# Kernel tuning notes

Measured on AMD Instinct MI355X. Metric: run time of the kernel, lower is better.

## Reference

```python
import jax, jax.numpy as jnp
import numpy as np

B, N, M = 8, 4096, 4096

def _sqdist(x, y):
    # x: [B,N,3], y: [B,M,3] -> squared euclidean distances [B,N,M]
    return jnp.sum((x[:, :, None, :] - y[:, None, :, :]) ** 2, axis=-1)

def _approx_match(xyz1, xyz2):
    # Faithful port of Fan et al. approxmatch.cu (used by PyTorchEMD's
    # earth_mover_distance): annealed soft-assignment over 10 levels.
    b, n, _ = xyz1.shape
    m = xyz2.shape[1]
    d2 = _sqdist(xyz1, xyz2)                      # [B,N,M]
    factorl = max(n, m) / n
    factorr = max(n, m) / m
    satl = jnp.full((b, n), factorl, d2.dtype)    # remaining mass, left
    satr = jnp.full((b, m), factorr, d2.dtype)    # remaining mass, right
    match = jnp.zeros_like(d2)
    # levels: -4^7 .. -4^-1, then 0 (exactly as in approxmatch.cu)
    levels = [-(4.0 ** j) for j in range(7, -2, -1)] + [0.0]
    for level in levels:
        w = jnp.exp(level * d2) * satr[:, None, :]                 # [B,N,M]
        w = w * (satl / (jnp.sum(w, axis=2) + 1e-9))[:, :, None]   # row normalize
        ss2 = jnp.sum(w, axis=1)                                   # [B,M]
        ratio = jnp.minimum(satr / (ss2 + 1e-9), 1.0)
        w = w * ratio[:, None, :]                                  # col capacity clamp
        match = match + w
        satl = jnp.maximum(satl - jnp.sum(w, axis=2), 0.0)
        satr = jnp.maximum(satr - ss2 * ratio, 0.0)
    return match, d2

def setup_inputs() -> dict:
    key = jax.random.key(0)
    k1, k2 = jax.random.split(key)
    array1 = jax.random.uniform(k1, (B, N, 3), dtype=jnp.float32)
    array2 = jax.random.uniform(k2, (B, M, 3), dtype=jnp.float32)
    return {"array1": array1, "array2": array2}

def reference(array1, array2):
    match, d2 = _approx_match(array1, array2)
    dist = jnp.sum(match * d2, axis=(1, 2))   # per-batch EMD (squared-dist transport cost), [B]
    return jnp.mean(dist) / array1.shape[1]
```

## Files before the change

### kernel.cpp

```cpp
#include <hip/hip_runtime.h>


#define BB 8
#define NN 4096
#define MM 4096
#define NPTS 4096

constexpr int   BLK   = 256;
constexpr int   S     = 16;
constexpr int   R     = 4;
constexpr int   RPB   = (BLK / S) * R;
constexpr int   CHUNK = 2048;
constexpr int   G     = (CHUNK / S) / 4;
constexpr float TAU   = 1e-8f;

#if defined(__has_builtin)
#if __has_builtin(__builtin_amdgcn_exp2f)
#define EXP2F(x) __builtin_amdgcn_exp2f(x)
#endif
#if __has_builtin(__builtin_amdgcn_logf)
#define LOG2F(x) __builtin_amdgcn_logf(x)
#endif
#endif
#ifndef EXP2F
#define EXP2F(x) exp2f(x)
#endif
#ifndef LOG2F
#define LOG2F(x) log2f(x)
#endif

__global__ void emd_sort(const float* __restrict__ xyz, float* __restrict__ xyzs) {
    __shared__ int hist[64];
    __shared__ int cur[64];
    const int b = blockIdx.x;
    const float* src = xyz + (size_t)b * NPTS * 3;
    float* dst = xyzs + (size_t)b * NPTS * 3;
    for (int i = threadIdx.x; i < 64; i += BLK) hist[i] = 0;
    __syncthreads();
    for (int i = threadIdx.x; i < NPTS; i += BLK) {
        float x = src[3*i], y = src[3*i+1], z = src[3*i+2];
        int cx = (int)(x * 4.0f); cx = cx < 0 ? 0 : (cx > 3 ? 3 : cx);
        int cy = (int)(y * 4.0f); cy = cy < 0 ? 0 : (cy > 3 ? 3 : cy);
        int cz = (int)(z * 4.0f); cz = cz < 0 ? 0 : (cz > 3 ? 3 : cz);
        atomicAdd(&hist[(cx << 4) | (cy << 2) | cz], 1);
    }
    __syncthreads();
    if (threadIdx.x == 0) {
        int acc = 0;
        for (int k = 0; k < 64; ++k) { cur[k] = acc; acc += hist[k]; }
    }
    __syncthreads();
    for (int i = threadIdx.x; i < NPTS; i += BLK) {
        float x = src[3*i], y = src[3*i+1], z = src[3*i+2];
        int cx = (int)(x * 4.0f); cx = cx < 0 ? 0 : (cx > 3 ? 3 : cx);
        int cy = (int)(y * 4.0f); cy = cy < 0 ? 0 : (cy > 3 ? 3 : cy);
        int cz = (int)(z * 4.0f); cz = cz < 0 ? 0 : (cz > 3 ? 3 : cz);
        int idx = atomicAdd(&cur[(cx << 4) | (cy << 2) | cz], 1);
        dst[3*idx] = x; dst[3*idx+1] = y; dst[3*idx+2] = z;
    }
}

__global__ void emd_bbox(const float* __restrict__ xyzs, float* __restrict__ bb,
                         int gp) {
    const int grp = blockIdx.x, lane = threadIdx.x;
    float xlo = 1e30f, xhi = -1e30f, ylo = 1e30f, yhi = -1e30f,
          zlo = 1e30f, zhi = -1e30f;
    if (lane < gp) {
        const float* p = xyzs + ((size_t)grp * gp + lane) * 3;
        xlo = xhi = p[0]; ylo = yhi = p[1]; zlo = zhi = p[2];
    }
    #pragma unroll
    for (int d = 1; d < 64; d <<= 1) {
        xlo = fminf(xlo, __shfl_xor(xlo, d)); xhi = fmaxf(xhi, __shfl_xor(xhi, d));
        ylo = fminf(ylo, __shfl_xor(ylo, d)); yhi = fmaxf(yhi, __shfl_xor(yhi, d));
        zlo = fminf(zlo, __shfl_xor(zlo, d)); zhi = fmaxf(zhi, __shfl_xor(zhi, d));
    }
    if (lane == 0) {
        float* o = bb + (size_t)grp * 6;
        o[0]=xlo; o[1]=xhi; o[2]=ylo; o[3]=yhi; o[4]=zlo; o[5]=zhi;
    }
}

__global__ void emd_init(float* __restrict__ satl, float* __restrict__ satr,
                         float* __restrict__ bsum, float* __restrict__ slsum,
                         float* __restrict__ scal, float* __restrict__ out) {
    int i = blockIdx.x * blockDim.x + threadIdx.x;
    if (i < BB * NN) satl[i] = 1.0f;
    if (i < BB * MM) satr[i] = 1.0f;
    if (i < BB)      bsum[i] = 0.0f;
    if (i < BB)      slsum[i] = 0.0f;
    if (i < BB * 5)  scal[i] = 0.0f;
    if (i == 0)      out[0]  = 0.0f;
}

__global__ void compact_rows(const float* __restrict__ xyzs,
                             const float* __restrict__ satl,
                             float* __restrict__ sl,
                             float4* __restrict__ rowBuf, int* __restrict__ rIdx,
                             int* __restrict__ rCnt) {
    __shared__ int cnts[BLK];
    const int b = blockIdx.x;
    const int PER = NN / BLK;
    const float* sb  = satl + (size_t)b * NN;
    float*       slb = sl   + (size_t)b * NN;
    const float* xb  = xyzs + (size_t)b * NN * 3;
    const int st = threadIdx.x * PER;
    int c = 0;
    for (int i = 0; i < PER; ++i) c += (sb[st + i] > TAU) ? 1 : 0;
    cnts[threadIdx.x] = c;
    __syncthreads();
    for (int d = 1; d < BLK; d <<= 1) {
        int v = cnts[threadIdx.x];
        int u = (threadIdx.x >= d) ? cnts[threadIdx.x - d] : 0;
        __syncthreads();
        cnts[threadIdx.x] = v + u;
        __syncthreads();
    }
    const int total = cnts[BLK - 1];
    int off = cnts[threadIdx.x] - c;
    for (int i = 0; i < PER; ++i) {
        int n = st + i;
        if (sb[n] > TAU) {
            rowBuf[(size_t)b * NN + off] =
                make_float4(xb[3*n], xb[3*n+1], xb[3*n+2], slb[n]);
            rIdx[(size_t)b * NN + off] = n;
            ++off;
        } else if (slb[n] != 0.0f) {
            slb[n] = 0.0f;
        }
    }
    for (int i = total + threadIdx.x; i < NN; i += BLK) {
        rowBuf[(size_t)b * NN + i] = make_float4(0.f, 0.f, 0.f, 0.f);
        rIdx[(size_t)b * NN + i] = 0;
    }
    if (threadIdx.x == 0) rCnt[b] = total;
}

__global__ void compact_cols(const float* __restrict__ xyzs,
                             const float* __restrict__ satr,
                             float4* __restrict__ colBuf, int* __restrict__ cIdx,
                             int* __restrict__ cCnt) {
    __shared__ int cnts[BLK];
    const int b = blockIdx.x;
    const int PER = MM / BLK;
    const float* sb = satr + (size_t)b * MM;
    const float* xb = xyzs + (size_t)b * MM * 3;
    const int st = threadIdx.x * PER;
    int c = 0;
    for (int i = 0; i < PER; ++i) c += (sb[st + i] > TAU) ? 1 : 0;
    cnts[threadIdx.x] = c;
    __syncthreads();
    for (int d = 1; d < BLK; d <<= 1) {
        int v = cnts[threadIdx.x];
        int u = (threadIdx.x >= d) ? cnts[threadIdx.x - d] : 0;
        __syncthreads();
        cnts[threadIdx.x] = v + u;
        __syncthreads();
    }
    const int total = cnts[BLK - 1];
    int off = cnts[threadIdx.x] - c;
    for (int i = 0; i < PER; ++i) {
        int m = st + i;
        if (sb[m] > TAU) {
            colBuf[(size_t)b * MM + off] =
                make_float4(xb[3*m], xb[3*m+1], xb[3*m+2], sb[m]);
            cIdx[(size_t)b * MM + off] = m;
            ++off;
        }
    }
    for (int i = total + threadIdx.x; i < MM; i += BLK) {
        colBuf[(size_t)b * MM + i] = make_float4(0.f, 0.f, 0.f, 0.f);
        cIdx[(size_t)b * MM + i] = 0;
    }
    if (threadIdx.x == 0) cCnt[b] = total;
}

#define AB_LOAD(vv, gg)                                          \
    _Pragma("unroll")                                            \
    for (int k = 0; k < 4; ++k) vv[k] = q[((gg)*4 + k)*S + s];

#define AB_COMP(vv)                                              \
    _Pragma("unroll")                                            \
    for (int k = 0; k < 4; ++k) {                                \
        float4 v = vv[k];                                        \
        _Pragma("unroll")                                        \
        for (int r = 0; r < R; ++r) {                            \
            float a0 = v.w + cpp[r];                             \
            float a1 = fmaf(zs[r], v.z, a0);                     \
            float a2 = fmaf(ys[r], v.y, a1);                     \
            float arg = fmaf(xs[r], v.x, a2);                    \
            acc[r] += EXP2F(arg);                                \
        }                                                        \
    }

#define RED_S(v)                                                 \
    v += __shfl_xor(v, 1);  v += __shfl_xor(v, 2);               \
    v += __shfl_xor(v, 4);  v += __shfl_xor(v, 8);

#define RED_W(v)                                                 \
    v += __shfl_xor(v, 1);  v += __shfl_xor(v, 2);               \
    v += __shfl_xor(v, 4);  v += __shfl_xor(v, 8);               \
    v += __shfl_xor(v, 16); v += __shfl_xor(v, 32);

#define BOX_SETUP(rbb)                                           \
    const float* rb = (rbb) + (size_t)(b * 256 + tile * 4 + (threadIdx.x >> 6)) * 6; \
    const float rx0 = rb[0], rx1 = rb[1], ry0 = rb[2], ry1 = rb[3], \
                rz0 = rb[4], rz1 = rb[5];

#define BOX_D2M(cbb, c0, gs, d2m)                                \
    const float* cb = (cbb) + (size_t)(b * 64 + ((c0) >> 6) + (gs)) * 6; \
    float gx = fmaxf(0.0f, fmaxf(cb[0] - rx1, rx0 - cb[1]));     \
    float gy = fmaxf(0.0f, fmaxf(cb[2] - ry1, ry0 - cb[3]));     \
    float gz = fmaxf(0.0f, fmaxf(cb[4] - rz1, rz0 - cb[5]));     \
    float d2m = fmaf(gx, gx, fmaf(gy, gy, gz * gz));

__global__ __launch_bounds__(BLK, 2) void emd_passA_p(
        const float* __restrict__ xyz1, const float* __restrict__ xyz2,
        const float* __restrict__ satl, const float* __restrict__ satr,
        float* __restrict__ sl, const float* __restrict__ rbb,
        const float* __restrict__ cbb, float c, float T) {
    __shared__ float4 q[CHUNK];
    const int b    = blockIdx.x / (NN / RPB);
    const int tile = blockIdx.x % (NN / RPB);
    const float* x2b = xyz2 + (size_t)b * MM * 3;
    const float* srb = satr + (size_t)b * MM;

    const int g = threadIdx.x / S, s = threadIdx.x % S;
    const int n0 = tile * RPB + g * R;
    const float* p = xyz1 + ((size_t)b * NN + n0) * 3;
    const float m2c = -2.0f * c;
    float xs[R], ys[R], zs[R], cpp[R], acc[R];
    #pragma unroll
    for (int r = 0; r < R; ++r) {
        float x = p[3*r], y = p[3*r+1], z = p[3*r+2];
        cpp[r] = c * (x*x + y*y + z*z);
        xs[r] = m2c * x; ys[r] = m2c * y; zs[r] = m2c * z;
        acc[r] = 0.0f;
    }
    BOX_SETUP(rbb);

    for (int c0 = 0; c0 < MM; c0 += CHUNK) {
        __syncthreads();
        for (int m = threadIdx.x; m < CHUNK; m += BLK) {
            int mm = c0 + m;
            float xx = x2b[3*mm], yy = x2b[3*mm+1], zz = x2b[3*mm+2];
            float qq = xx*xx + yy*yy + zz*zz;
            q[m] = make_float4(xx, yy, zz, fmaf(c, qq, LOG2F(srb[mm])));
        }
        __syncthreads();
        for (int gs = 0; gs < G; ++gs) {
            BOX_D2M(cbb, c0, gs, d2m);
            if (d2m > T) continue;
            float4 va[4];
            AB_LOAD(va, gs);
            AB_COMP(va);
        }
    }
    #pragma unroll
    for (int r = 0; r < R; ++r) { RED_S(acc[r]); }
    if (s == 0) {
        #pragma unroll
        for (int r = 0; r < R; ++r) {
            int gi = b * NN + n0 + r;
            sl[gi] = satl[gi] / (acc[r] + 1e-9f);
        }
    }
}

__global__ __launch_bounds__(BLK, 2) void emd_passB_p(
        const float* __restrict__ xyz1, const float* __restrict__ xyz2,
        const float* __restrict__ sl, float* __restrict__ satr,
        float* __restrict__ sr2, const float* __restrict__ rbb,
        const float* __restrict__ cbb, float c, float T) {
    __shared__ float4 q[CHUNK];
    const int b    = blockIdx.x / (MM / RPB);
    const int tile = blockIdx.x % (MM / RPB);
    const float* x1b = xyz1 + (size_t)b * NN * 3;
    const float* slb = sl + (size_t)b * NN;

    const int g = threadIdx.x / S, s = threadIdx.x % S;
    const int m0 = tile * RPB + g * R;
    const float* qp = xyz2 + ((size_t)b * MM + m0) * 3;
    const float m2c = -2.0f * c;
    float xs[R], ys[R], zs[R], cpp[R], acc[R];
    #pragma unroll
    for (int r = 0; r < R; ++r) {
        float x = qp[3*r], y = qp[3*r+1], z = qp[3*r+2];
        cpp[r] = c * (x*x + y*y + z*z);
        xs[r] = m2c * x; ys[r] = m2c * y; zs[r] = m2c * z;
        acc[r] = 0.0f;
    }
    BOX_SETUP(rbb);

    for (int c0 = 0; c0 < NN; c0 += CHUNK) {
        __syncthreads();
        for (int n = threadIdx.x; n < CHUNK; n += BLK) {
            int nn = c0 + n;
            float xx = x1b[3*nn], yy = x1b[3*nn+1], zz = x1b[3*nn+2];
            float pp = xx*xx + yy*yy + zz*zz;
            q[n] = make_float4(xx, yy, zz, fmaf(c, pp, LOG2F(slb[nn])));
        }
        __syncthreads();
        for (int gs = 0; gs < G; ++gs) {
            BOX_D2M(cbb, c0, gs, d2m);
            if (d2m > T) continue;
            float4 va[4];
            AB_LOAD(va, gs);
            AB_COMP(va);
        }
    }
    #pragma unroll
    for (int r = 0; r < R; ++r) { RED_S(acc[r]); }
    if (s == 0) {
        #pragma unroll
        for (int r = 0; r < R; ++r) {
            int gi = b * MM + m0 + r;
            float sr    = satr[gi];
            float ss2   = acc[r] * sr;
            float ratio = fminf(sr / (ss2 + 1e-9f), 1.0f);
            float sn    = fmaxf(sr - ss2 * ratio, 0.0f);
            sr2[gi]  = sr * ratio;
            satr[gi] = sn;
        }
    }
}

#define CA0_LOAD(vv, ww, gg)                                     \
    _Pragma("unroll")                                            \
    for (int k = 0; k < 4; ++k) {                                \
        int idx = ((gg)*4 + k)*S + s;                            \
        vv[k] = q[idx]; ww[k] = w[idx];                          \
    }

#define CA0_COMP(vv, ww)                                         \
    _Pragma("unroll")                                            \
    for (int k = 0; k < 4; ++k) {                                \
        float4 v = vv[k]; float2 wv = ww[k];                     \
        _Pragma("unroll")                                        \
        for (int r = 0; r < R; ++r) {                            \
            float a0 = v.w + cnpp[r];                            \
            float a1 = fmaf(zs[r], v.z, a0);                     \
            float a2 = fmaf(ys[r], v.y, a1);                     \
            float arg = fmaf(xs[r], v.x, a2);                    \
            float en  = EXP2F(arg);                              \
            acc2[r] = fmaf(en, wv.y, acc2[r]);                   \
            float e2 = en * en;                                  \
            float t  = (e2 * e2) * wv.x;                         \
            rd[r]   += t;                                        \
            costA[r] = fmaf(t, arg, costA[r]);                   \
        }                                                        \
    }

__global__ __launch_bounds__(BLK, 2) void emd_passCA0_p(
        const float* __restrict__ xyz1, const float* __restrict__ xyz2,
        float* __restrict__ sl, float* __restrict__ satl,
        const float* __restrict__ sr2, const float* __restrict__ satr_next,
        float* __restrict__ out, const float* __restrict__ rbb,
        const float* __restrict__ cbb, float cl, float cn, float T) {
    __shared__ float4 q[CHUNK];
    __shared__ float2 w[CHUNK];
    const int b    = blockIdx.x / (NN / RPB);
    const int tile = blockIdx.x % (NN / RPB);
    const float* x2b = xyz2 + (size_t)b * MM * 3;
    const float* s2b = sr2 + (size_t)b * MM;
    const float* srb = satr_next + (size_t)b * MM;

    const int g = threadIdx.x / S, s = threadIdx.x % S;
    const int n0 = tile * RPB + g * R;
    const float* pp_ = xyz1 + ((size_t)b * NN + n0) * 3;
    const float m2cn = -2.0f * cn;
    const float icn  = 1.0f / cn;
    float xs[R], ys[R], zs[R], cnpp[R], rd[R], costA[R], acc2[R], slv[R];
    #pragma unroll
    for (int r = 0; r < R; ++r) {
        float x = pp_[3*r], y = pp_[3*r+1], z = pp_[3*r+2];
        cnpp[r] = cn * (x*x + y*y + z*z);
        xs[r] = m2cn * x; ys[r] = m2cn * y; zs[r] = m2cn * z;
        rd[r] = 0.0f; costA[r] = 0.0f; acc2[r] = 0.0f;
        slv[r] = sl[b * NN + n0 + r];
    }
    BOX_SETUP(rbb);

    for (int c0 = 0; c0 < MM; c0 += CHUNK) {
        __syncthreads();
        for (int m = threadIdx.x; m < CHUNK; m += BLK) {
            int mm = c0 + m;
            float xx = x2b[3*mm], yy = x2b[3*mm+1], zz = x2b[3*mm+2];
            float qq = xx*xx + yy*yy + zz*zz;
            q[m] = make_float4(xx, yy, zz, cn * qq);
            w[m] = make_float2(s2b[mm], srb[mm]);
        }
        __syncthreads();
        for (int gs = 0; gs < G; ++gs) {
            BOX_D2M(cbb, c0, gs, d2m);
            if (d2m > T) continue;
            float4 va[4]; float2 wa[4];
            CA0_LOAD(va, wa, gs);
            CA0_COMP(va, wa);
        }
    }

    #pragma unroll
    for (int r = 0; r < R; ++r) { RED_S(rd[r]); RED_S(acc2[r]); }

    float csum = 0.0f;
    #pragma unroll
    for (int r = 0; r < R; ++r) csum += (costA[r] * icn) * slv[r];
    RED_W(csum);
    if ((threadIdx.x & 63) == 0)
        atomicAdd(out, csum * (1.0f / (float)(BB * NN)));

    if (s == 0) {
        #pragma unroll
        for (int r = 0; r < R; ++r) {
            int gi = b * NN + n0 + r;
            float sa = fmaxf(satl[gi] - rd[r] * slv[r], 0.0f);
            satl[gi] = sa;
            sl[gi] = sa / (acc2[r] + 1e-9f);
        }
    }
}

__global__ __launch_bounds__(BLK, 2) void emd_passB_c(
        const float4* __restrict__ colBuf, const int* __restrict__ cIdx,
        const int* __restrict__ cCnt, const float4* __restrict__ rowBuf,
        const int* __restrict__ rCnt, float* __restrict__ satr,
        float* __restrict__ sr2c, float* __restrict__ satrnc,
        float* __restrict__ bsum, int do_sum, float c) {
    __shared__ float4 q[CHUNK];
    const int b    = blockIdx.x / (MM / RPB);
    const int tile = blockIdx.x % (MM / RPB);
    const int Mc = cCnt[b], Nc = rCnt[b];
    if (tile * RPB >= Mc) return;
    const float4* rb = rowBuf + (size_t)b * NN;

    const int g = threadIdx.x / S, s = threadIdx.x % S;
    const int m0 = tile * RPB + g * R;
    const float m2c = -2.0f * c;
    float xs[R], ys[R], zs[R], cpp[R], acc[R], srv[R];
    #pragma unroll
    for (int r = 0; r < R; ++r) {
        float4 cv = colBuf[(size_t)b * MM + m0 + r];
        srv[r] = cv.w;
        cpp[r] = c * (cv.x*cv.x + cv.y*cv.y + cv.z*cv.z);
        xs[r] = m2c * cv.x; ys[r] = m2c * cv.y; zs[r] = m2c * cv.z;
        acc[r] = 0.0f;
    }

    const int nch = (Nc + CHUNK - 1) / CHUNK;
    for (int ci = 0; ci < nch; ++ci) {
        const int c0 = ci * CHUNK;
        __syncthreads();
        for (int n = threadIdx.x; n < CHUNK; n += BLK) {
            int nn = c0 + n;
            if (nn < Nc) {
                float4 rv = rb[nn];
                float pp = rv.x*rv.x + rv.y*rv.y + rv.z*rv.z;
                q[n] = make_float4(rv.x, rv.y, rv.z, fmaf(c, pp, LOG2F(rv.w)));
            } else {
                q[n] = make_float4(0.f, 0.f, 0.f, -1e30f);
            }
        }
        __syncthreads();
        int rem = Nc - c0; if (rem > CHUNK) rem = CHUNK;
        const int Gact = (rem + S*4 - 1) / (S*4);
        float4 va[4], vb[4];
        AB_LOAD(va, 0);
        #pragma unroll 1
        for (int gs = 0; gs < Gact; gs += 2) {
            if (gs + 1 < Gact) { AB_LOAD(vb, gs + 1); }
            AB_COMP(va);
            if (gs + 2 < Gact) { AB_LOAD(va, gs + 2); }
            if (gs + 1 < Gact) { AB_COMP(vb); }
        }
    }
    #pragma unroll
    for (int r = 0; r < R; ++r) { RED_S(acc[r]); }
    float part = 0.0f;
    if (s == 0) {
        #pragma unroll
        for (int r = 0; r < R; ++r) {
            if (m0 + r < Mc) {
                float sr    = srv[r];
                float ss2   = acc[r] * sr;
                float ratio = fminf(sr / (ss2 + 1e-9f), 1.0f);
                float sn    = fmaxf(sr - ss2 * ratio, 0.0f);
                size_t ci2 = (size_t)b * MM + m0 + r;
                sr2c[ci2]   = sr * ratio;
                satrnc[ci2] = sn;
                satr[(size_t)b * MM + cIdx[ci2]] = sn;
                part += sn;
            }
        }
    }
    if (do_sum) {
        RED_W(part);
        if ((threadIdx.x & 63) == 0) atomicAdd(&bsum[b], part);
    }
}

__global__ __launch_bounds__(BLK, 2) void emd_passCA0_c(
        const float4* __restrict__ rowBuf, const int* __restrict__ rIdx,
        const int* __restrict__ rCnt, const float4* __restrict__ colBuf,
        const int* __restrict__ cCnt, const float* __restrict__ sr2c,
        const float* __restrict__ satrnc, float* __restrict__ satl,
        float* __restrict__ sl, float* __restrict__ out, float cl, float cn) {
    __shared__ float4 q[CHUNK];
    __shared__ float2 w[CHUNK];
    const int b    = blockIdx.x / (NN / RPB);
    const int tile = blockIdx.x % (NN / RPB);
    const int Nc = rCnt[b], Mc = cCnt[b];
    if (tile * RPB >= Nc) return;
    const float4* cbp = colBuf + (size_t)b * MM;
    const float* s2p = sr2c + (size_t)b * MM;
    const float* snp = satrnc + (size_t)b * MM;

    const int g = threadIdx.x / S, s = threadIdx.x % S;
    const int n0 = tile * RPB + g * R;
    const float m2cn = -2.0f * cn;
    const float icn  = 1.0f / cn;
    float xs[R], ys[R], zs[R], cnpp[R], rd[R], costA[R], acc2[R], slv[R];
    #pragma unroll
    for (int r = 0; r < R; ++r) {
        float4 rv = rowBuf[(size_t)b * NN + n0 + r];
        slv[r] = rv.w;
        cnpp[r] = cn * (rv.x*rv.x + rv.y*rv.y + rv.z*rv.z);
        xs[r] = m2cn * rv.x; ys[r] = m2cn * rv.y; zs[r] = m2cn * rv.z;
        rd[r] = 0.0f; costA[r] = 0.0f; acc2[r] = 0.0f;
    }

    const int nch = (Mc + CHUNK - 1) / CHUNK;
    for (int ci = 0; ci < nch; ++ci) {
        const int c0 = ci * CHUNK;
        __syncthreads();
        for (int m = threadIdx.x; m < CHUNK; m += BLK) {
            int mm = c0 + m;
            if (mm < Mc) {
                float4 cv = cbp[mm];
                float qq = cv.x*cv.x + cv.y*cv.y + cv.z*cv.z;
                q[m] = make_float4(cv.x, cv.y, cv.z, cn * qq);
                w[m] = make_float2(s2p[mm], snp[mm]);
            } else {
                q[m] = make_float4(0.f, 0.f, 0.f, 0.f);
                w[m] = make_float2(0.f, 0.f);
            }
        }
        __syncthreads();
        int rem = Mc - c0; if (rem > CHUNK) rem = CHUNK;
        const int Gact = (rem + S*4 - 1) / (S*4);
        float4 va[4], vb[4]; float2 wa[4], wb[4];
        CA0_LOAD(va, wa, 0);
        #pragma unroll 1
        for (int gs = 0; gs < Gact; gs += 2) {
            if (gs + 1 < Gact) { CA0_LOAD(vb, wb, gs + 1); }
            CA0_COMP(va, wa);
            if (gs + 2 < Gact) { CA0_LOAD(va, wa, gs + 2); }
            if (gs + 1 < Gact) { CA0_COMP(vb, wb); }
        }
    }

    #pragma unroll
    for (int r = 0; r < R; ++r) { RED_S(rd[r]); RED_S(acc2[r]); }

    float csum = 0.0f;
    #pragma unroll
    for (int r = 0; r < R; ++r) csum += (costA[r] * icn) * slv[r];
    RED_W(csum);
    if ((threadIdx.x & 63) == 0)
        atomicAdd(out, csum * (1.0f / (float)(BB * NN)));

    if (s == 0) {
        #pragma unroll
        for (int r = 0; r < R; ++r) {
            if (n0 + r < Nc) {
                int gi = b * NN + rIdx[(size_t)b * NN + n0 + r];
                float sa = fmaxf(satl[gi] - rd[r] * slv[r], 0.0f);
                satl[gi] = sa;
                sl[gi] = sa / (acc2[r] + 1e-9f);
            }
        }
    }
}

#define CA1_LOAD(vv, aa, gg)                                     \
    _Pragma("unroll")                                            \
    for (int k = 0; k < 4; ++k) {                                \
        int idx = ((gg)*4 + k)*S + s;                            \
        vv[k] = q[idx]; aa[k] = qa[idx];                         \
    }

#define CA1_COMP(vv, aa)                                         \
    _Pragma("unroll")                                            \
    for (int k = 0; k < 4; ++k) {                                \
        float4 v = vv[k]; float lw = aa[k];                      \
        _Pragma("unroll")                                        \
        for (int r = 0; r < R; ++r) {                            \
            float a0 = v.w + clpp[r];                            \
            float a1 = fmaf(zs[r], v.z, a0);                     \
            float a2 = fmaf(ys[r], v.y, a1);                     \
            float arg = fmaf(xs[r], v.x, a2);                    \
            float t   = EXP2F(arg);                              \
            rd[r] += t;                                          \
            c1[r] = fmaf(t, arg, c1[r]);                         \
            c2[r] = fmaf(t, lw, c2[r]);                          \
        }                                                        \
    }

__global__ __launch_bounds__(BLK, 2) void emd_passCA1_c(
        const float4* __restrict__ rowBuf, const int* __restrict__ rIdx,
        const int* __restrict__ rCnt, const float4* __restrict__ colBuf,
        const int* __restrict__ cCnt, const float* __restrict__ sr2c,
        float* __restrict__ satl, float* __restrict__ sl,
        const float* __restrict__ bsum, float* __restrict__ slsum,
        float* __restrict__ out, float cl) {
    __shared__ float4 q[CHUNK];
    __shared__ float  qa[CHUNK];
    const int b    = blockIdx.x / (NN / RPB);
    const int tile = blockIdx.x % (NN / RPB);
    const int Nc = rCnt[b], Mc = cCnt[b];
    if (tile * RPB >= Nc) return;
    const float4* cbp = colBuf + (size_t)b * MM;
    const float* s2p = sr2c + (size_t)b * MM;

    const int g = threadIdx.x / S, s = threadIdx.x % S;
    const int n0 = tile * RPB + g * R;
    const float m2cl = -2.0f * cl;
    const float icl  = 1.0f / cl;
    float xs[R], ys[R], zs[R], clpp[R], rd[R], c1[R], c2[R], slv[R];
    #pragma unroll
    for (int r = 0; r < R; ++r) {
        float4 rv = rowBuf[(size_t)b * NN + n0 + r];
        slv[r] = rv.w;
        clpp[r] = cl * (rv.x*rv.x + rv.y*rv.y + rv.z*rv.z);
        xs[r] = m2cl * rv.x; ys[r] = m2cl * rv.y; zs[r] = m2cl * rv.z;
        rd[r] = 0.0f; c1[r] = 0.0f; c2[r] = 0.0f;
    }

    const int nch = (Mc + CHUNK - 1) / CHUNK;
    for (int ci = 0; ci < nch; ++ci) {
        const int c0 = ci * CHUNK;
        __syncthreads();
        for (int m = threadIdx.x; m < CHUNK; m += BLK) {
            int mm = c0 + m;
            if (mm < Mc) {
                float4 cv = cbp[mm];
                float qq = cv.x*cv.x + cv.y*cv.y + cv.z*cv.z;
                float lw = LOG2F(fmaxf(s2p[mm], 1e-30f));
                q[m]  = make_float4(cv.x, cv.y, cv.z, fmaf(cl, qq, lw));
                qa[m] = lw;
            } else {
                q[m]  = make_float4(0.f, 0.f, 0.f, -1e30f);
                qa[m] = 0.f;
            }
        }
        __syncthreads();
        int rem = Mc - c0; if (rem > CHUNK) rem = CHUNK;
        const int Gact = (rem + S*4 - 1) / (S*4);
        float4 va[4], vb[4]; float aa[4], ab[4];
        CA1_LOAD(va, aa, 0);
        #pragma unroll 1
        for (int gs = 0; gs < Gact; gs += 2) {
            if (gs + 1 < Gact) { CA1_LOAD(vb, ab, gs + 1); }
            CA1_COMP(va, aa);
            if (gs + 2 < Gact) { CA1_LOAD(va, aa, gs + 2); }
            if (gs + 1 < Gact) { CA1_COMP(vb, ab); }
        }
    }

    #pragma unroll
    for (int r = 0; r < R; ++r) { RED_S(rd[r]); }

    float csum = 0.0f;
    #pragma unroll
    for (int r = 0; r < R; ++r) csum += ((c1[r] - c2[r]) * icl) * slv[r];
    RED_W(csum);
    if ((threadIdx.x & 63) == 0)
        atomicAdd(out, csum * (1.0f / (float)(BB * NN)));

    float part = 0.0f;
    if (s == 0) {
        float bs = bsum[b];
        #pragma unroll
        for (int r = 0; r < R; ++r) {
            if (n0 + r < Nc) {
                int gi = b * NN + rIdx[(size_t)b * NN + n0 + r];
                float sa = fmaxf(satl[gi] - rd[r] * slv[r], 0.0f);
                satl[gi] = sa;
                float s9 = sa / (bs + 1e-9f);
                sl[gi] = s9;
                part += s9;
            }
        }
    }
    RED_W(part);
    if ((threadIdx.x & 63) == 0) atomicAdd(&slsum[b], part);
}

__global__ void emd_lvl9_col(const float* __restrict__ xyz2,
                             const float* __restrict__ satr,
                             const float* __restrict__ slsum,
                             float* __restrict__ scal) {
    int i = blockIdx.x * blockDim.x + threadIdx.x;
    int b = i / MM;
    const float* qp = xyz2 + (size_t)i * 3;
    float sr = satr[i];
    float ss2 = sr * slsum[b];
    float ratio = fminf(sr / (ss2 + 1e-9f), 1.0f);
    float s2 = sr * ratio;
    float x = qp[0], y = qp[1], z = qp[2];
    float v0 = s2, v1 = s2*x, v2 = s2*y, v3 = s2*z;
    float v4 = s2 * (x*x + y*y + z*z);
    #pragma unroll
    for (int d = 1; d < 64; d <<= 1) {
        v0 += __shfl_xor(v0, d); v1 += __shfl_xor(v1, d);
        v2 += __shfl_xor(v2, d); v3 += __shfl_xor(v3, d);
        v4 += __shfl_xor(v4, d);
    }
    if ((threadIdx.x & 63) == 0) {
        atomicAdd(&scal[b*5+0], v0); atomicAdd(&scal[b*5+1], v1);
        atomicAdd(&scal[b*5+2], v2); atomicAdd(&scal[b*5+3], v3);
        atomicAdd(&scal[b*5+4], v4);
    }
}

__global__ void emd_lvl9_cost(const float* __restrict__ xyz1,
                              const float* __restrict__ sl,
                              const float* __restrict__ scal,
                              float* __restrict__ out) {
    int i = blockIdx.x * blockDim.x + threadIdx.x;
    int b = i / NN;
    float W  = scal[b*5+0], Wx = scal[b*5+1], Wy = scal[b*5+2];
    float Wz = scal[b*5+3], Q  = scal[b*5+4];
    const float* p = xyz1 + (size_t)i * 3;
    float x = p[0], y = p[1], z = p[2];
    float pp = x*x + y*y + z*z;
    float dotw = x*Wx + y*Wy + z*Wz;
    float c = sl[i] * (pp * W + Q - 2.0f * dotw);
    #pragma unroll
    for (int d = 1; d < 64; d <<= 1) c += __shfl_xor(c, d);
    if ((threadIdx.x & 63) == 0)
        atomicAdd(out, c * (1.0f / (float)(BB * NN)));
}

extern "C" void kernel_launch(void* const* d_in, const int* in_sizes, int n_in,
                              void* d_out, int out_size, void* d_ws, size_t ws_size,
                              hipStream_t stream) {
    const float* xyz1 = (const float*)d_in[0];
    const float* xyz2 = (const float*)d_in[1];
    float* out  = (float*)d_out;

    float* satl   = (float*)d_ws;
    float* sl     = satl  + BB * NN;
    float* satr   = sl    + BB * NN;
    float* sr2    = satr  + BB * MM;
    float* bsum   = sr2   + BB * MM;
    float* slsum  = bsum  + BB;
    float* scal   = slsum + BB;
    float* xyz1s  = scal  + BB * 5;
    float* xyz2s  = xyz1s + BB * NN * 3;
    float* bb1_16 = xyz2s + BB * MM * 3;
    float* bb1_64 = bb1_16 + BB * 256 * 6;
    float* bb2_16 = bb1_64 + BB * 64 * 6;
    float* bb2_64 = bb2_16 + BB * 256 * 6;
    float4* rowBuf = (float4*)(bb2_64 + BB * 64 * 6);
    float4* colBuf = rowBuf + BB * NN;
    float* sr2c   = (float*)(colBuf + BB * MM);
    float* satrnc = sr2c  + BB * MM;
    int*   rIdx   = (int*)(satrnc + BB * MM);
    int*   cIdx   = rIdx  + BB * NN;
    int*   rCnt   = cIdx  + BB * MM;
    int*   cCnt   = rCnt  + BB;

    emd_sort<<<BB, BLK, 0, stream>>>(xyz1, xyz1s);
    emd_sort<<<BB, BLK, 0, stream>>>(xyz2, xyz2s);
    emd_bbox<<<BB * (NN / 16), 64, 0, stream>>>(xyz1s, bb1_16, 16);
    emd_bbox<<<BB * (NN / 64), 64, 0, stream>>>(xyz1s, bb1_64, 64);
    emd_bbox<<<BB * (MM / 16), 64, 0, stream>>>(xyz2s, bb2_16, 16);
    emd_bbox<<<BB * (MM / 64), 64, 0, stream>>>(xyz2s, bb2_64, 64);
    emd_init<<<(BB * NN + 255) / 256, 256, 0, stream>>>(satl, satr, bsum,
                                                        slsum, scal, out);

    const double levels[10] = {-16384.0, -4096.0, -1024.0, -256.0, -64.0,
                               -16.0, -4.0, -1.0, -0.25, 0.0};
    const double LOG2E = 1.4426950408889634;
    float c[10], T[10];
    for (int l = 0; l < 10; ++l) {
        c[l] = (float)(levels[l] * LOG2E);
        T[l] = (l < 9) ? (float)(80.0 / (-levels[l] * LOG2E)) : 1e30f;
    }

    const int grid = BB * (NN / RPB);

    emd_passA_p<<<grid, BLK, 0, stream>>>(xyz1s, xyz2s, satl, satr, sl,
                                          bb1_16, bb2_64, c[0], T[0]);
    for (int l = 0; l <= 2; ++l) {
        emd_passB_p<<<grid, BLK, 0, stream>>>(xyz1s, xyz2s, sl, satr, sr2,
                                              bb2_16, bb1_64, c[l], T[l]);
        emd_passCA0_p<<<grid, BLK, 0, stream>>>(
            xyz1s, xyz2s, sl, satl, sr2, satr, out, bb1_16, bb2_64,
            c[l], c[l + 1], T[l + 1]);
    }

    compact_cols<<<BB, BLK, 0, stream>>>(xyz2s, satr, colBuf, cIdx, cCnt);
    compact_rows<<<BB, BLK, 0, stream>>>(xyz1s, satl, sl, rowBuf, rIdx, rCnt);
    for (int l = 3; l <= 8; ++l) {
        emd_passB_c<<<grid, BLK, 0, stream>>>(colBuf, cIdx, cCnt, rowBuf, rCnt,
                                              satr, sr2c, satrnc, bsum,
                                              (l == 8) ? 1 : 0, c[l]);
        if (l < 8) {
            emd_passCA0_c<<<grid, BLK, 0, stream>>>(
                rowBuf, rIdx, rCnt, colBuf, cCnt, sr2c, satrnc,
                satl, sl, out, c[l], c[l + 1]);
            compact_cols<<<BB, BLK, 0, stream>>>(xyz2s, satr, colBuf, cIdx, cCnt);
            compact_rows<<<BB, BLK, 0, stream>>>(xyz1s, satl, sl, rowBuf, rIdx, rCnt);
        } else {
            emd_passCA1_c<<<grid, BLK, 0, stream>>>(
                rowBuf, rIdx, rCnt, colBuf, cCnt, sr2c,
                satl, sl, bsum, slsum, out, c[8]);
        }
    }
    emd_lvl9_col<<<BB * MM / 256, 256, 0, stream>>>(xyz2s, satr, slsum, scal);
    emd_lvl9_cost<<<BB * NN / 256, 256, 0, stream>>>(xyz1s, sl, scal, out);
}
```

Before: 775.4 us.

## Add finer 16-point box culling in pruned passes and merge small setup kernels

Adds a second level of bounding-box culling inside the pruned passes A, B and CA0. Each 64-point column group that survives the coarse test is now checked per 16-point sub-box, skipping exp work for sub-boxes beyond the threshold. It also merges the sort, bbox and row/column compaction launches into single kernels to cut launch count. The finer test adds per-sub-box global loads and branches and gives up the batched 4-wide load pattern, which may reduce ILP.

```diff
diff --git a/kernel.cpp b/kernel.cpp
--- a/kernel.cpp
+++ b/kernel.cpp
@@ -29,12 +29,15 @@
 #define LOG2F(x) log2f(x)
 #endif
 
-__global__ void emd_sort(const float* __restrict__ xyz, float* __restrict__ xyzs) {
+__global__ void emd_sort(const float* __restrict__ x1, const float* __restrict__ x2,
+                         float* __restrict__ s1, float* __restrict__ s2) {
     __shared__ int hist[64];
     __shared__ int cur[64];
-    const int b = blockIdx.x;
-    const float* src = xyz + (size_t)b * NPTS * 3;
-    float* dst = xyzs + (size_t)b * NPTS * 3;
+    const int blk = blockIdx.x;
+    const float* src = (blk < BB) ? x1 + (size_t)blk * NPTS * 3
+                                  : x2 + (size_t)(blk - BB) * NPTS * 3;
+    float* dst = (blk < BB) ? s1 + (size_t)blk * NPTS * 3
+                            : s2 + (size_t)(blk - BB) * NPTS * 3;
     for (int i = threadIdx.x; i < 64; i += BLK) hist[i] = 0;
     __syncthreads();
     for (int i = threadIdx.x; i < NPTS; i += BLK) {
@@ -60,13 +63,22 @@
     }
 }
 
-__global__ void emd_bbox(const float* __restrict__ xyzs, float* __restrict__ bb,
-                         int gp) {
-    const int grp = blockIdx.x, lane = threadIdx.x;
+__global__ void emd_bbox_all(const float* __restrict__ x1s,
+                             const float* __restrict__ x2s,
+                             float* __restrict__ bb1_16, float* __restrict__ bb1_64,
+                             float* __restrict__ bb2_16, float* __restrict__ bb2_64) {
+    const int PER = BB * 256 + BB * 64;
+    int id = blockIdx.x;
+    int cloud = id / PER, r = id % PER;
+    const float* xs = cloud ? x2s : x1s;
+    float* bb; int gp, grp;
+    if (r < BB * 256) { gp = 16; grp = r; bb = cloud ? bb2_16 : bb1_16; }
+    else             { gp = 64; grp = r - BB * 256; bb = cloud ? bb2_64 : bb1_64; }
+    const int lane = threadIdx.x;
     float xlo = 1e30f, xhi = -1e30f, ylo = 1e30f, yhi = -1e30f,
           zlo = 1e30f, zhi = -1e30f;
     if (lane < gp) {
-        const float* p = xyzs + ((size_t)grp * gp + lane) * 3;
+        const float* p = xs + ((size_t)grp * gp + lane) * 3;
         xlo = xhi = p[0]; ylo = yhi = p[1]; zlo = zhi = p[2];
     }
     #pragma unroll
@@ -93,17 +105,22 @@
     if (i == 0)      out[0]  = 0.0f;
 }
 
-__global__ void compact_rows(const float* __restrict__ xyzs,
-                             const float* __restrict__ satl,
-                             float* __restrict__ sl,
-                             float4* __restrict__ rowBuf, int* __restrict__ rIdx,
-                             int* __restrict__ rCnt) {
+__global__ void compact_all(const float* __restrict__ xyz1s,
+                            const float* __restrict__ xyz2s,
+                            const float* __restrict__ satl,
+                            const float* __restrict__ satr,
+                            float* __restrict__ sl,
+                            float4* __restrict__ rowBuf, int* __restrict__ rIdx,
+                            int* __restrict__ rCnt,
+                            float4* __restrict__ colBuf, int* __restrict__ cIdx,
+                            int* __restrict__ cCnt) {
     __shared__ int cnts[BLK];
-    const int b = blockIdx.x;
-    const int PER = NN / BLK;
-    const float* sb  = satl + (size_t)b * NN;
-    float*       slb = sl   + (size_t)b * NN;
-    const float* xb  = xyzs + (size_t)b * NN * 3;
+    const bool isRow = blockIdx.x >= BB;
+    const int b = isRow ? (blockIdx.x - BB) : blockIdx.x;
+    const int PER = NPTS / BLK;
+    const float* sb = (isRow ? satl : satr) + (size_t)b * NPTS;
+    const float* xb = (isRow ? xyz1s : xyz2s) + (size_t)b * NPTS * 3;
+    float* slb = sl + (size_t)b * NN;
     const int st = threadIdx.x * PER;
     int c = 0;
     for (int i = 0; i < PER; ++i) c += (sb[st + i] > TAU) ? 1 : 0;
@@ -118,61 +135,39 @@
     }
     const int total = cnts[BLK - 1];
     int off = cnts[threadIdx.x] - c;
-    for (int i = 0; i < PER; ++i) {
-        int n = st + i;
-        if (sb[n] > TAU) {
-            rowBuf[(size_t)b * NN + off] =
-                make_float4(xb[3*n], xb[3*n+1], xb[3*n+2], slb[n]);
-            rIdx[(size_t)b * NN + off] = n;
-            ++off;
-        } else if (slb[n] != 0.0f) {
-            slb[n] = 0.0f;
-        }
-    }
-    for (int i = total + threadIdx.x; i < NN; i += BLK) {
-        rowBuf[(size_t)b * NN + i] = make_float4(0.f, 0.f, 0.f, 0.f);
-        rIdx[(size_t)b * NN + i] = 0;
-    }
-    if (threadIdx.x == 0) rCnt[b] = total;
-}
-
-__global__ void compact_cols(const float* __restrict__ xyzs,
-                             const float* __restrict__ satr,
-                             float4* __restrict__ colBuf, int* __restrict__ cIdx,
-                             int* __restrict__ cCnt) {
-    __shared__ int cnts[BLK];
-    const int b = blockIdx.x;
-    const int PER = MM / BLK;
-    const float* sb = satr + (size_t)b * MM;
-    const float* xb = xyzs + (size_t)b * MM * 3;
-    const int st = threadIdx.x * PER;
-    int c = 0;
-    for (int i = 0; i < PER; ++i) c += (sb[st + i] > TAU) ? 1 : 0;
-    cnts[threadIdx.x] = c;
-    __syncthreads();
-    for (int d = 1; d < BLK; d <<= 1) {
-        int v = cnts[threadIdx.x];
-        int u = (threadIdx.x >= d) ? cnts[threadIdx.x - d] : 0;
-        __syncthreads();
-        cnts[threadIdx.x] = v + u;
-        __syncthreads();
-    }
-    const int total = cnts[BLK - 1];
-    int off = cnts[threadIdx.x] - c;
-    for (int i = 0; i < PER; ++i) {
-        int m = st + i;
-        if (sb[m] > TAU) {
-            colBuf[(size_t)b * MM + off] =
-                make_float4(xb[3*m], xb[3*m+1], xb[3*m+2], sb[m]);
-            cIdx[(size_t)b * MM + off] = m;
-            ++off;
-        }
-    }
-    for (int i = total + threadIdx.x; i < MM; i += BLK) {
-        colBuf[(size_t)b * MM + i] = make_float4(0.f, 0.f, 0.f, 0.f);
-        cIdx[(size_t)b * MM + i] = 0;
-    }
-    if (threadIdx.x == 0) cCnt[b] = total;
+    if (isRow) {
+        for (int i = 0; i < PER; ++i) {
+            int n = st + i;
+            if (sb[n] > TAU) {
+                rowBuf[(size_t)b * NN + off] =
+                    make_float4(xb[3*n], xb[3*n+1], xb[3*n+2], slb[n]);
+                rIdx[(size_t)b * NN + off] = n;
+                ++off;
+            } else if (slb[n] != 0.0f) {
+                slb[n] = 0.0f;
+            }
+        }
+        for (int i = total + threadIdx.x; i < NN; i += BLK) {
+            rowBuf[(size_t)b * NN + i] = make_float4(0.f, 0.f, 0.f, 0.f);
+            rIdx[(size_t)b * NN + i] = 0;
+        }
+        if (threadIdx.x == 0) rCnt[b] = total;
+    } else {
+        for (int i = 0; i < PER; ++i) {
+            int m = st + i;
+            if (sb[m] > TAU) {
+                colBuf[(size_t)b * MM + off] =
+                    make_float4(xb[3*m], xb[3*m+1], xb[3*m+2], sb[m]);
+                cIdx[(size_t)b * MM + off] = m;
+                ++off;
+            }
+        }
+        for (int i = total + threadIdx.x; i < MM; i += BLK) {
+            colBuf[(size_t)b * MM + i] = make_float4(0.f, 0.f, 0.f, 0.f);
+            cIdx[(size_t)b * MM + i] = 0;
+        }
+        if (threadIdx.x == 0) cCnt[b] = total;
+    }
 }
 
 #define AB_LOAD(vv, gg)                                          \
@@ -193,6 +188,16 @@
         }                                                        \
     }
 
+#define AB_COMP1(v)                                              \
+    { _Pragma("unroll")                                          \
+      for (int r = 0; r < R; ++r) {                              \
+        float a0 = (v).w + cpp[r];                               \
+        float a1 = fmaf(zs[r], (v).z, a0);                       \
+        float a2 = fmaf(ys[r], (v).y, a1);                       \
+        float arg = fmaf(xs[r], (v).x, a2);                      \
+        acc[r] += EXP2F(arg);                                    \
+      } }
+
 #define RED_S(v)                                                 \
     v += __shfl_xor(v, 1);  v += __shfl_xor(v, 2);               \
     v += __shfl_xor(v, 4);  v += __shfl_xor(v, 8);
@@ -214,11 +219,19 @@
     float gz = fmaxf(0.0f, fmaxf(cb[4] - rz1, rz0 - cb[5]));     \
     float d2m = fmaf(gx, gx, fmaf(gy, gy, gz * gz));
 
+#define BOX_D2M16(cbb16, c0, gs, k, dd)                          \
+    const float* cb2 = (cbb16) + (size_t)(b * 256 + ((c0) >> 4) + (gs)*4 + (k)) * 6; \
+    float hx = fmaxf(0.0f, fmaxf(cb2[0] - rx1, rx0 - cb2[1]));   \
+    float hy = fmaxf(0.0f, fmaxf(cb2[2] - ry1, ry0 - cb2[3]));   \
+    float hz = fmaxf(0.0f, fmaxf(cb2[4] - rz1, rz0 - cb2[5]));   \
+    float dd = fmaf(hx, hx, fmaf(hy, hy, hz * hz));
+
 __global__ __launch_bounds__(BLK, 2) void emd_passA_p(
         const float* __restrict__ xyz1, const float* __restrict__ xyz2,
         const float* __restrict__ satl, const float* __restrict__ satr,
         float* __restrict__ sl, const float* __restrict__ rbb,
-        const float* __restrict__ cbb, float c, float T) {
+        const float* __restrict__ cbb, const float* __restrict__ cbb16,
+        float c, float T) {
     __shared__ float4 q[CHUNK];
     const int b    = blockIdx.x / (NN / RPB);
     const int tile = blockIdx.x % (NN / RPB);
@@ -251,9 +264,13 @@
         for (int gs = 0; gs < G; ++gs) {
             BOX_D2M(cbb, c0, gs, d2m);
             if (d2m > T) continue;
-            float4 va[4];
-            AB_LOAD(va, gs);
-            AB_COMP(va);
+            #pragma unroll
+            for (int k = 0; k < 4; ++k) {
+                BOX_D2M16(cbb16, c0, gs, k, dd);
+                if (dd > T) continue;
+                float4 v = q[(gs*4 + k)*S + s];
+                AB_COMP1(v);
+            }
         }
     }
     #pragma unroll
@@ -271,7 +288,8 @@
         const float* __restrict__ xyz1, const float* __restrict__ xyz2,
         const float* __restrict__ sl, float* __restrict__ satr,
         float* __restrict__ sr2, const float* __restrict__ rbb,
-        const float* __restrict__ cbb, float c, float T) {
+        const float* __restrict__ cbb, const float* __restrict__ cbb16,
+        float c, float T) {
     __shared__ float4 q[CHUNK];
     const int b    = blockIdx.x / (MM / RPB);
     const int tile = blockIdx.x % (MM / RPB);
@@ -304,9 +322,13 @@
         for (int gs = 0; gs < G; ++gs) {
             BOX_D2M(cbb, c0, gs, d2m);
             if (d2m > T) continue;
-            float4 va[4];
-            AB_LOAD(va, gs);
-            AB_COMP(va);
+            #pragma unroll
+            for (int k = 0; k < 4; ++k) {
+                BOX_D2M16(cbb16, c0, gs, k, dd);
+                if (dd > T) continue;
+                float4 v = q[(gs*4 + k)*S + s];
+                AB_COMP1(v);
+            }
         }
     }
     #pragma unroll
@@ -351,12 +373,28 @@
         }                                                        \
     }
 
+#define CA0_COMP1(v, wv)                                         \
+    { _Pragma("unroll")                                          \
+      for (int r = 0; r < R; ++r) {                              \
+        float a0 = (v).w + cnpp[r];                              \
+        float a1 = fmaf(zs[r], (v).z, a0);                       \
+        float a2 = fmaf(ys[r], (v).y, a1);                       \
+        float arg = fmaf(xs[r], (v).x, a2);                      \
+        float en  = EXP2F(arg);                                  \
+        acc2[r] = fmaf(en, (wv).y, acc2[r]);                     \
+        float e2 = en * en;                                      \
+        float t  = (e2 * e2) * (wv).x;                           \
+        rd[r]   += t;                                            \
+        costA[r] = fmaf(t, arg, costA[r]);                       \
+      } }
+
 __global__ __launch_bounds__(BLK, 2) void emd_passCA0_p(
         const float* __restrict__ xyz1, const float* __restrict__ xyz2,
         float* __restrict__ sl, float* __restrict__ satl,
         const float* __restrict__ sr2, const float* __restrict__ satr_next,
         float* __restrict__ out, const float* __restrict__ rbb,
-        const float* __restrict__ cbb, float cl, float cn, float T) {
+        const float* __restrict__ cbb, const float* __restrict__ cbb16,
+        float cl, float cn, float T) {
     __shared__ float4 q[CHUNK];
     __shared__ float2 w[CHUNK];
     const int b    = blockIdx.x / (NN / RPB);
@@ -394,9 +432,15 @@
         for (int gs = 0; gs < G; ++gs) {
             BOX_D2M(cbb, c0, gs, d2m);
             if (d2m > T) continue;
-            float4 va[4]; float2 wa[4];
-            CA0_LOAD(va, wa, gs);
-            CA0_COMP(va, wa);
+            #pragma unroll
+            for (int k = 0; k < 4; ++k) {
+                BOX_D2M16(cbb16, c0, gs, k, dd);
+                if (dd > T) continue;
+                int idx = (gs*4 + k)*S + s;
+                float4 v  = q[idx];
+                float2 wv = w[idx];
+                CA0_COMP1(v, wv);
+            }
         }
     }
 
@@ -771,12 +815,9 @@
     int*   rCnt   = cIdx  + BB * MM;
     int*   cCnt   = rCnt  + BB;
 
-    emd_sort<<<BB, BLK, 0, stream>>>(xyz1, xyz1s);
-    emd_sort<<<BB, BLK, 0, stream>>>(xyz2, xyz2s);
-    emd_bbox<<<BB * (NN / 16), 64, 0, stream>>>(xyz1s, bb1_16, 16);
-    emd_bbox<<<BB * (NN / 64), 64, 0, stream>>>(xyz1s, bb1_64, 64);
-    emd_bbox<<<BB * (MM / 16), 64, 0, stream>>>(xyz2s, bb2_16, 16);
-    emd_bbox<<<BB * (MM / 64), 64, 0, stream>>>(xyz2s, bb2_64, 64);
+    emd_sort<<<2 * BB, BLK, 0, stream>>>(xyz1, xyz2, xyz1s, xyz2s);
+    emd_bbox_all<<<2 * (BB * 256 + BB * 64), 64, 0, stream>>>(
+        xyz1s, xyz2s, bb1_16, bb1_64, bb2_16, bb2_64);
     emd_init<<<(BB * NN + 255) / 256, 256, 0, stream>>>(satl, satr, bsum,
                                                         slsum, scal, out);
 
@@ -792,17 +833,18 @@
     const int grid = BB * (NN / RPB);
 
     emd_passA_p<<<grid, BLK, 0, stream>>>(xyz1s, xyz2s, satl, satr, sl,
-                                          bb1_16, bb2_64, c[0], T[0]);
+                                          bb1_16, bb2_64, bb2_16, c[0], T[0]);
     for (int l = 0; l <= 2; ++l) {
         emd_passB_p<<<grid, BLK, 0, stream>>>(xyz1s, xyz2s, sl, satr, sr2,
-                                              bb2_16, bb1_64, c[l], T[l]);
+                                              bb2_16, bb1_64, bb1_16, c[l], T[l]);
         emd_passCA0_p<<<grid, BLK, 0, stream>>>(
-            xyz1s, xyz2s, sl, satl, sr2, satr, out, bb1_16, bb2_64,
+            xyz1s, xyz2s, sl, satl, sr2, satr, out, bb1_16, bb2_64, bb2_16,
             c[l], c[l + 1], T[l + 1]);
     }
 
-    compact_cols<<<BB, BLK, 0, stream>>>(xyz2s, satr, colBuf, cIdx, cCnt);
-    compact_rows<<<BB, BLK, 0, stream>>>(xyz1s, satl, sl, rowBuf, rIdx, rCnt);
+    compact_all<<<2 * BB, BLK, 0, stream>>>(xyz1s, xyz2s, satl, satr, sl,
+                                            rowBuf, rIdx, rCnt,
+                                            colBuf, cIdx, cCnt);
     for (int l = 3; l <= 8; ++l) {
         emd_passB_c<<<grid, BLK, 0, stream>>>(colBuf, cIdx, cCnt, rowBuf, rCnt,
                                               satr, sr2c, satrnc, bsum,
@@ -811,8 +853,9 @@
             emd_passCA0_c<<<grid, BLK, 0, stream>>>(
                 rowBuf, rIdx, rCnt, colBuf, cCnt, sr2c, satrnc,
                 satl, sl, out, c[l], c[l + 1]);
-            compact_cols<<<BB, BLK, 0, stream>>>(xyz2s, satr, colBuf, cIdx, cCnt);
-            compact_rows<<<BB, BLK, 0, stream>>>(xyz1s, satl, sl, rowBuf, rIdx, rCnt);
+            compact_all<<<2 * BB, BLK, 0, stream>>>(xyz1s, xyz2s, satl, satr, sl,
+                                                    rowBuf, rIdx, rCnt,
+                                                    colBuf, cIdx, cCnt);
         } else {
             emd_passCA1_c<<<grid, BLK, 0, stream>>>(
                 rowBuf, rIdx, rCnt, colBuf, cCnt, sr2c,
```

After: 882.5 us. +13.8%, slower.
